# Kernel tuning notes

Hardware: AMD Instinct MI355X
Metric: run time of the kernel (lower is better)

## Reference

```python
import jax, jax.numpy as jnp
import numpy as np

B, L, D, H = 2, 2048, 1024, 16
DH = D // H  # 64


def setup_inputs() -> dict:
    key = jax.random.key(0)
    ks = jax.random.split(key, 11)
    s = 0.02
    return {
        "src": jax.random.normal(ks[0], (B, L, D), dtype=jnp.float32),
        "Wq": jax.random.normal(ks[1], (D, D), dtype=jnp.float32) * s,
        "bq": jax.random.normal(ks[2], (D,), dtype=jnp.float32) * s,
        "Wk": jax.random.normal(ks[3], (D, D), dtype=jnp.float32) * s,
        "bk": jax.random.normal(ks[4], (D,), dtype=jnp.float32) * s,
        "Wv": jax.random.normal(ks[5], (D, D), dtype=jnp.float32) * s,
        "bv": jax.random.normal(ks[6], (D,), dtype=jnp.float32) * s,
        "Wo": jax.random.normal(ks[7], (D, D), dtype=jnp.float32) * s,
        "bo": jax.random.normal(ks[8], (D,), dtype=jnp.float32) * s,
        "conv_w": jax.random.normal(ks[9], (H, D, 3), dtype=jnp.float32) * s,  # Conv1d weight [out=H, in=D, k=3]
        "conv_b": jax.random.normal(ks[10], (H,), dtype=jnp.float32) * s,
    }


def reference(src, Wq, bq, Wk, bk, Wv, bv, Wo, bo, conv_w, conv_b):
    b, l, d = src.shape
    h, dh = H, DH
    # QKV projections (torch Linear: x @ W.T + b), split into heads: [B,H,L,DH]
    Q = (src @ Wq.T + bq).reshape(b, l, h, dh).transpose(0, 2, 1, 3)
    K = (src @ Wk.T + bk).reshape(b, l, h, dh).transpose(0, 2, 1, 3)
    V = (src @ Wv.T + bv).reshape(b, l, h, dh).transpose(0, 2, 1, 3)
    # saliency conv: Conv1d(D->H, k=3, padding='same') on [B,D,L] -> [B,H,L]
    sal = jax.lax.conv_general_dilated(
        src.transpose(0, 2, 1), conv_w,
        window_strides=(1,), padding=[(1, 1)],
        dimension_numbers=("NCH", "OIH", "NCH"),
    ) + conv_b[None, :, None]
    # attention scores + per-head saliency bias (broadcast over query axis)
    scores = jnp.einsum("bhqd,bhkd->bhqk", Q, K) / jnp.sqrt(jnp.float32(dh))
    scores = scores + sal[:, :, None, :]
    attn = jax.nn.softmax(scores, axis=-1)  # dropout is identity in eval
    out = jnp.einsum("bhqk,bhkd->bhqd", attn, V)  # [B,H,L,DH]
    out = out.transpose(0, 2, 1, 3).reshape(b, l, d)
    out = out @ Wo.T + bo
    return out, attn
```

## Files before the change

kernel.cpp:

```cpp
#include <hip/hip_runtime.h>

typedef __bf16 bf16x8 __attribute__((ext_vector_type(8)));
typedef float f32x4 __attribute__((ext_vector_type(4)));
typedef unsigned short u16;
typedef unsigned int u32;

#define MFMA(a, b, c) __builtin_amdgcn_mfma_f32_16x16x32_bf16((a), (b), (c), 0, 0, 0)


__device__ __forceinline__ u16 f2bf(float f) {
  u32 u = __float_as_uint(f);
  return (u16)((u + 0x7fffu + ((u >> 16) & 1u)) >> 16);
}

__global__ __launch_bounds__(256) void cvt_bf16(const float4* __restrict__ x,
                                                uint2* __restrict__ y, int n4) {
  int i = blockIdx.x * 256 + threadIdx.x;
  if (i >= n4) return;
  float4 v = x[i];
  uint2 o;
  o.x = (u32)f2bf(v.x) | ((u32)f2bf(v.y) << 16);
  o.y = (u32)f2bf(v.z) | ((u32)f2bf(v.w) << 16);
  y[i] = o;
}

__global__ __launch_bounds__(256) void prep_cw(const float* __restrict__ cw,
                                               float* __restrict__ cwT) {
  int i = blockIdx.x * 256 + threadIdx.x;
  if (i >= 16 * 3 * 1024) return;
  int h = i / 3072;
  int j = (i - h * 3072) >> 10;
  int d = i & 1023;
  cwT[i] = cw[(h * 1024 + d) * 3 + j];
}

__global__ __launch_bounds__(256) void conv_sal_k(const float* __restrict__ src,
                                                  const float* __restrict__ cwT,
                                                  const float* __restrict__ cb,
                                                  float* __restrict__ sal) {
  const int t = threadIdx.x;
  const int h = t & 15, li = t >> 4;
  const int b = blockIdx.y;
  const int l = blockIdx.x * 16 + li;
  float acc = cb[h];
#pragma unroll
  for (int j = 0; j < 3; j++) {
    int ls = l + j - 1;
    if (ls < 0 || ls >= 2048) continue;
    const float4* sp = (const float4*)(src + ((size_t)b * 2048 + ls) * 1024);
    const float4* wp = (const float4*)(cwT + (h * 3 + j) * 1024);
    float s = 0.f;
    for (int d = 0; d < 256; d++) {
      float4 a = sp[d], w = wp[d];
      s += a.x * w.x + a.y * w.y + a.z * w.z + a.w * w.w;
    }
    acc += s;
  }
  sal[(b * 16 + h) * 2048 + l] = acc;
}

__global__ __launch_bounds__(256) void qkv_gemm(
    const u16* __restrict__ Xb, const u16* __restrict__ Wqb, const u16* __restrict__ Wkb,
    const u16* __restrict__ Wvb, const float* __restrict__ bq, const float* __restrict__ bk,
    const float* __restrict__ bv, u16* __restrict__ Qb, u16* __restrict__ Kb,
    u16* __restrict__ Vt) {
  const int seg = blockIdx.x >> 3;
  const u16* __restrict__ W = (seg == 0) ? Wqb : (seg == 1) ? Wkb : Wvb;
  const float* __restrict__ bias = (seg == 0) ? bq : (seg == 1) ? bk : bv;
  const int lane = threadIdx.x & 63, wid = threadIdx.x >> 6;
  const int cl = lane & 15, gp = lane >> 4;
  const int m0 = blockIdx.y * 128 + (wid >> 1) * 64;
  const int n0 = (blockIdx.x & 7) * 128 + (wid & 1) * 64;
  const u16* Xp = Xb + (size_t)(m0 + cl) * 1024 + gp * 8;
  const u16* Wp = W + (size_t)(n0 + cl) * 1024 + gp * 8;
  f32x4 acc[4][4] = {};
  for (int k = 0; k < 1024; k += 32) {
    bf16x8 a[4], b[4];
#pragma unroll
    for (int t = 0; t < 4; t++) {
      a[t] = *(const bf16x8*)(Xp + t * 16 * 1024 + k);
      b[t] = *(const bf16x8*)(Wp + t * 16 * 1024 + k);
    }
#pragma unroll
    for (int tm = 0; tm < 4; tm++)
#pragma unroll
      for (int tn = 0; tn < 4; tn++) acc[tm][tn] = MFMA(a[tm], b[tn], acc[tm][tn]);
  }
#pragma unroll
  for (int tn = 0; tn < 4; tn++) {
    int col = n0 + tn * 16 + cl;
    float bv_ = bias[col];
    int hh = col >> 6, dh = col & 63;
#pragma unroll
    for (int tm = 0; tm < 4; tm++) {
#pragma unroll
      for (int r = 0; r < 4; r++) {
        int row = m0 + tm * 16 + gp * 4 + r;
        u16 hv = f2bf(acc[tm][tn][r] + bv_);
        int bb = row >> 11, l = row & 2047;
        if (seg == 0)
          Qb[(((size_t)(bb * 16 + hh) * 2048 + l) << 6) + dh] = hv;
        else if (seg == 1)
          Kb[(((size_t)(bb * 16 + hh) * 2048 + l) << 6) + dh] = hv;
        else
          Vt[((size_t)(bb * 16 + hh) * 64 + dh) * 2048 + l] = hv;
      }
    }
  }
}

__global__ __launch_bounds__(256) void out_gemm(const u16* __restrict__ Xb,
                                                const u16* __restrict__ W,
                                                const float* __restrict__ bias,
                                                float* __restrict__ Y) {
  const int lane = threadIdx.x & 63, wid = threadIdx.x >> 6;
  const int cl = lane & 15, gp = lane >> 4;
  const int m0 = blockIdx.y * 128 + (wid >> 1) * 64;
  const int n0 = blockIdx.x * 128 + (wid & 1) * 64;
  const u16* Xp = Xb + (size_t)(m0 + cl) * 1024 + gp * 8;
  const u16* Wp = W + (size_t)(n0 + cl) * 1024 + gp * 8;
  f32x4 acc[4][4] = {};
  for (int k = 0; k < 1024; k += 32) {
    bf16x8 a[4], b[4];
#pragma unroll
    for (int t = 0; t < 4; t++) {
      a[t] = *(const bf16x8*)(Xp + t * 16 * 1024 + k);
      b[t] = *(const bf16x8*)(Wp + t * 16 * 1024 + k);
    }
#pragma unroll
    for (int tm = 0; tm < 4; tm++)
#pragma unroll
      for (int tn = 0; tn < 4; tn++) acc[tm][tn] = MFMA(a[tm], b[tn], acc[tm][tn]);
  }
#pragma unroll
  for (int tn = 0; tn < 4; tn++) {
    int col = n0 + tn * 16 + cl;
    float bv_ = bias[col];
#pragma unroll
    for (int tm = 0; tm < 4; tm++)
#pragma unroll
      for (int r = 0; r < 4; r++) {
        int row = m0 + tm * 16 + gp * 4 + r;
        Y[(size_t)row * 1024 + col] = acc[tm][tn][r] + bv_;
      }
  }
}

__global__ __launch_bounds__(256) void flash1(const u16* __restrict__ Qb,
                                              const u16* __restrict__ Kb,
                                              const u16* __restrict__ Vt,
                                              const float* __restrict__ sal,
                                              float* __restrict__ mrow,
                                              float* __restrict__ invl,
                                              u16* __restrict__ Ob) {
  __shared__ __align__(16) u16 pbuf[4][16][72];
  const int bh = blockIdx.x;
  const int b = bh >> 4, h = bh & 15;
  const int lane = threadIdx.x & 63, wid = threadIdx.x >> 6;
  const int cl = lane & 15, gp = lane >> 4;
  const int q0 = blockIdx.y * 64 + wid * 16;
  const u16* Qh = Qb + (size_t)bh * 2048 * 64;
  const u16* Kh = Kb + (size_t)bh * 2048 * 64;
  const u16* Vh = Vt + (size_t)bh * 64 * 2048;
  const float* salh = sal + bh * 2048;
  bf16x8 aQ0 = *(const bf16x8*)(Qh + (size_t)(q0 + cl) * 64 + gp * 8);
  bf16x8 aQ1 = *(const bf16x8*)(Qh + (size_t)(q0 + cl) * 64 + 32 + gp * 8);
  f32x4 oacc[4] = {};
  float m[4], l[4];
#pragma unroll
  for (int r = 0; r < 4; r++) { m[r] = -1e30f; l[r] = 0.f; }
  u16* pw = &pbuf[wid][0][0];
  for (int kb = 0; kb < 2048; kb += 64) {
    f32x4 st[4];
#pragma unroll
    for (int tn = 0; tn < 4; tn++) {
      const u16* kp = Kh + (size_t)(kb + tn * 16 + cl) * 64 + gp * 8;
      f32x4 s = {};
      s = MFMA(aQ0, *(const bf16x8*)kp, s);
      s = MFMA(aQ1, *(const bf16x8*)(kp + 32), s);
      st[tn] = s;
    }
#pragma unroll
    for (int tn = 0; tn < 4; tn++) {
      float sv = salh[kb + tn * 16 + cl];
#pragma unroll
      for (int r = 0; r < 4; r++) st[tn][r] = st[tn][r] * 0.125f + sv;
    }
    float mn[4], alpha[4];
#pragma unroll
    for (int r = 0; r < 4; r++) {
      float v = fmaxf(fmaxf(st[0][r], st[1][r]), fmaxf(st[2][r], st[3][r]));
      v = fmaxf(v, __shfl_xor(v, 1));
      v = fmaxf(v, __shfl_xor(v, 2));
      v = fmaxf(v, __shfl_xor(v, 4));
      v = fmaxf(v, __shfl_xor(v, 8));
      mn[r] = fmaxf(m[r], v);
      alpha[r] = __expf(m[r] - mn[r]);
      m[r] = mn[r];
    }
#pragma unroll
    for (int r = 0; r < 4; r++) {
      float s0 = 0.f;
#pragma unroll
      for (int tn = 0; tn < 4; tn++) {
        float p = __expf(st[tn][r] - mn[r]);
        st[tn][r] = p;
        s0 += p;
      }
      s0 += __shfl_xor(s0, 1);
      s0 += __shfl_xor(s0, 2);
      s0 += __shfl_xor(s0, 4);
      s0 += __shfl_xor(s0, 8);
      l[r] = l[r] * alpha[r] + s0;
#pragma unroll
      for (int tn = 0; tn < 4; tn++) oacc[tn][r] *= alpha[r];
    }
#pragma unroll
    for (int tn = 0; tn < 4; tn++)
#pragma unroll
      for (int r = 0; r < 4; r++) pw[(gp * 4 + r) * 72 + tn * 16 + cl] = f2bf(st[tn][r]);
    __syncthreads();
    bf16x8 aP0 = *(const bf16x8*)(pw + cl * 72 + gp * 8);
    bf16x8 aP1 = *(const bf16x8*)(pw + cl * 72 + 32 + gp * 8);
#pragma unroll
    for (int tn = 0; tn < 4; tn++) {
      const u16* vp = Vh + (size_t)(tn * 16 + cl) * 2048 + kb + gp * 8;
      oacc[tn] = MFMA(aP0, *(const bf16x8*)vp, oacc[tn]);
      oacc[tn] = MFMA(aP1, *(const bf16x8*)(vp + 32), oacc[tn]);
    }
    __syncthreads();
  }
  float inv[4];
#pragma unroll
  for (int r = 0; r < 4; r++) inv[r] = 1.0f / l[r];
#pragma unroll
  for (int tn = 0; tn < 4; tn++) {
    int d = h * 64 + tn * 16 + cl;
#pragma unroll
    for (int r = 0; r < 4; r++) {
      int q = q0 + gp * 4 + r;
      Ob[((size_t)(b * 2048 + q)) * 1024 + d] = f2bf(oacc[tn][r] * inv[r]);
    }
  }
  if (cl == 0) {
#pragma unroll
    for (int r = 0; r < 4; r++) {
      int q = q0 + gp * 4 + r;
      mrow[bh * 2048 + q] = m[r];
      invl[bh * 2048 + q] = inv[r];
    }
  }
}

__global__ __launch_bounds__(256) void attn_write(const u16* __restrict__ Qb,
                                                  const u16* __restrict__ Kb,
                                                  const float* __restrict__ sal,
                                                  const float* __restrict__ mrow,
                                                  const float* __restrict__ invl,
                                                  float* __restrict__ attn) {
  const int bh = blockIdx.x;
  const int lane = threadIdx.x & 63, wid = threadIdx.x >> 6;
  const int cl = lane & 15, gp = lane >> 4;
  const int q0 = blockIdx.y * 64 + wid * 16;
  const u16* Qh = Qb + (size_t)bh * 2048 * 64;
  const u16* Kh = Kb + (size_t)bh * 2048 * 64;
  const float* salh = sal + bh * 2048;
  bf16x8 aQ0 = *(const bf16x8*)(Qh + (size_t)(q0 + cl) * 64 + gp * 8);
  bf16x8 aQ1 = *(const bf16x8*)(Qh + (size_t)(q0 + cl) * 64 + 32 + gp * 8);
  float m[4], il[4];
#pragma unroll
  for (int r = 0; r < 4; r++) {
    int q = q0 + gp * 4 + r;
    m[r] = mrow[bh * 2048 + q];
    il[r] = invl[bh * 2048 + q];
  }
  float* arow = attn + (size_t)bh * 2048 * 2048;
  for (int kb = 0; kb < 2048; kb += 64) {
    f32x4 st[4];
#pragma unroll
    for (int tn = 0; tn < 4; tn++) {
      const u16* kp = Kh + (size_t)(kb + tn * 16 + cl) * 64 + gp * 8;
      f32x4 s = {};
      s = MFMA(aQ0, *(const bf16x8*)kp, s);
      s = MFMA(aQ1, *(const bf16x8*)(kp + 32), s);
      st[tn] = s;
    }
#pragma unroll
    for (int tn = 0; tn < 4; tn++) {
      float sv = salh[kb + tn * 16 + cl];
#pragma unroll
      for (int r = 0; r < 4; r++) {
        int q = q0 + gp * 4 + r;
        float p = __expf(st[tn][r] * 0.125f + sv - m[r]) * il[r];
        arow[(size_t)q * 2048 + kb + tn * 16 + cl] = p;
      }
    }
  }
}

extern "C" void kernel_launch(void* const* d_in, const int* in_sizes, int n_in,
                              void* d_out, int out_size, void* d_ws, size_t ws_size,
                              hipStream_t stream) {
  const float* src = (const float*)d_in[0];
  const float* Wq = (const float*)d_in[1];
  const float* bq = (const float*)d_in[2];
  const float* Wk = (const float*)d_in[3];
  const float* bk = (const float*)d_in[4];
  const float* Wv = (const float*)d_in[5];
  const float* bv = (const float*)d_in[6];
  const float* Wo = (const float*)d_in[7];
  const float* bo = (const float*)d_in[8];
  const float* cw = (const float*)d_in[9];
  const float* cb = (const float*)d_in[10];

  char* ws = (char*)d_ws;
  u16* srcb = (u16*)(ws + 0);
  u16* wqb = (u16*)(ws + 8388608);
  u16* wkb = (u16*)(ws + 10485760);
  u16* wvb = (u16*)(ws + 12582912);
  u16* wob = (u16*)(ws + 14680064);
  u16* Qb = (u16*)(ws + 16777216);
  u16* Kb = (u16*)(ws + 25165824);
  u16* Vt = (u16*)(ws + 33554432);
  u16* Ob = (u16*)(ws + 41943040);
  float* cwT = (float*)(ws + 50331648);
  float* sal = (float*)(ws + 50528256);
  float* mrow = (float*)(ws + 50790400);
  float* invl = (float*)(ws + 51052544);

  float* outp = (float*)d_out;
  float* attn = (float*)d_out + 4194304;

  cvt_bf16<<<4096, 256, 0, stream>>>((const float4*)src, (uint2*)srcb, 1048576);
  cvt_bf16<<<1024, 256, 0, stream>>>((const float4*)Wq, (uint2*)wqb, 262144);
  cvt_bf16<<<1024, 256, 0, stream>>>((const float4*)Wk, (uint2*)wkb, 262144);
  cvt_bf16<<<1024, 256, 0, stream>>>((const float4*)Wv, (uint2*)wvb, 262144);
  cvt_bf16<<<1024, 256, 0, stream>>>((const float4*)Wo, (uint2*)wob, 262144);
  prep_cw<<<192, 256, 0, stream>>>(cw, cwT);
  conv_sal_k<<<dim3(128, 2), 256, 0, stream>>>(src, cwT, cb, sal);
  qkv_gemm<<<dim3(24, 32), 256, 0, stream>>>(srcb, wqb, wkb, wvb, bq, bk, bv, Qb, Kb, Vt);
  flash1<<<dim3(32, 32), 256, 0, stream>>>(Qb, Kb, Vt, sal, mrow, invl, Ob);
  attn_write<<<dim3(32, 32), 256, 0, stream>>>(Qb, Kb, sal, mrow, invl, attn);
  out_gemm<<<dim3(8, 32), 256, 0, stream>>>(Ob, wob, bo, outp);
}
```

Before: 1.164 ms.

## Fuse prep kernels, stage GEMM tiles in LDS, merge flash and attn-write passes

Merges the five bf16 conversion kernels and the conv-weight transpose into one launch. The QKV and output GEMMs now load tiles cooperatively into shared memory instead of each wave reading global memory directly. The two attention kernels become one two-pass kernel: the first pass finds row max and sum, the second writes normalized attention and accumulates P·V, which drops one QK pass and the mrow/invl round trip. The conv accumulator is also split into four lanes; the GEMM LDS staging adds two barriers per k-step with no double buffering.

```diff
diff --git a/kernel.cpp b/kernel.cpp
--- a/kernel.cpp
+++ b/kernel.cpp
@@ -13,25 +13,35 @@
   return (u16)((u + 0x7fffu + ((u >> 16) & 1u)) >> 16);
 }
 
-__global__ __launch_bounds__(256) void cvt_bf16(const float4* __restrict__ x,
-                                                uint2* __restrict__ y, int n4) {
-  int i = blockIdx.x * 256 + threadIdx.x;
-  if (i >= n4) return;
-  float4 v = x[i];
-  uint2 o;
-  o.x = (u32)f2bf(v.x) | ((u32)f2bf(v.y) << 16);
-  o.y = (u32)f2bf(v.z) | ((u32)f2bf(v.w) << 16);
-  y[i] = o;
-}
-
-__global__ __launch_bounds__(256) void prep_cw(const float* __restrict__ cw,
-                                               float* __restrict__ cwT) {
-  int i = blockIdx.x * 256 + threadIdx.x;
-  if (i >= 16 * 3 * 1024) return;
-  int h = i / 3072;
-  int j = (i - h * 3072) >> 10;
-  int d = i & 1023;
-  cwT[i] = cw[(h * 1024 + d) * 3 + j];
+__global__ __launch_bounds__(256) void prep_all(
+    const float4* __restrict__ src, const float4* __restrict__ wq,
+    const float4* __restrict__ wk, const float4* __restrict__ wv,
+    const float4* __restrict__ wo, const float* __restrict__ cw,
+    uint2* __restrict__ srcb, uint2* __restrict__ wqb, uint2* __restrict__ wkb,
+    uint2* __restrict__ wvb, uint2* __restrict__ wob, float* __restrict__ cwT) {
+  int bx = blockIdx.x;
+  if (bx < 8192) {
+    const float4* in;
+    uint2* out;
+    int base;
+    if (bx < 4096) { in = src; out = srcb; base = 0; }
+    else if (bx < 5120) { in = wq; out = wqb; base = 4096; }
+    else if (bx < 6144) { in = wk; out = wkb; base = 5120; }
+    else if (bx < 7168) { in = wv; out = wvb; base = 6144; }
+    else { in = wo; out = wob; base = 7168; }
+    int i = (bx - base) * 256 + threadIdx.x;
+    float4 v = in[i];
+    uint2 o;
+    o.x = (u32)f2bf(v.x) | ((u32)f2bf(v.y) << 16);
+    o.y = (u32)f2bf(v.z) | ((u32)f2bf(v.w) << 16);
+    out[i] = o;
+  } else {
+    int i = (bx - 8192) * 256 + threadIdx.x;
+    int h = i / 3072;
+    int j = (i - h * 3072) >> 10;
+    int d = i & 1023;
+    cwT[i] = cw[(h * 1024 + d) * 3 + j];
+  }
 }
 
 __global__ __launch_bounds__(256) void conv_sal_k(const float* __restrict__ src,
@@ -42,21 +52,59 @@
   const int h = t & 15, li = t >> 4;
   const int b = blockIdx.y;
   const int l = blockIdx.x * 16 + li;
-  float acc = cb[h];
+  float4 acc = {0.f, 0.f, 0.f, 0.f};
 #pragma unroll
   for (int j = 0; j < 3; j++) {
     int ls = l + j - 1;
     if (ls < 0 || ls >= 2048) continue;
     const float4* sp = (const float4*)(src + ((size_t)b * 2048 + ls) * 1024);
     const float4* wp = (const float4*)(cwT + (h * 3 + j) * 1024);
-    float s = 0.f;
     for (int d = 0; d < 256; d++) {
       float4 a = sp[d], w = wp[d];
-      s += a.x * w.x + a.y * w.y + a.z * w.z + a.w * w.w;
-    }
-    acc += s;
-  }
-  sal[(b * 16 + h) * 2048 + l] = acc;
+      acc.x += a.x * w.x;
+      acc.y += a.y * w.y;
+      acc.z += a.z * w.z;
+      acc.w += a.w * w.w;
+    }
+  }
+  sal[(b * 16 + h) * 2048 + l] = cb[h] + ((acc.x + acc.y) + (acc.z + acc.w));
+}
+
+__device__ __forceinline__ void gemm_core(const u16* __restrict__ Xg, const u16* __restrict__ Wg,
+                                          int mblk, int nblk, u16* smA, u16* smB,
+                                          f32x4 acc[4][4]) {
+  const int t = threadIdx.x;
+  const int lane = t & 63, wid = t >> 6;
+  const int cl = lane & 15, gp = lane >> 4;
+  const int r0 = t >> 2, cc = (t & 3) * 8;
+  const u16* gA0 = Xg + (size_t)(mblk + r0) * 1024 + cc;
+  const u16* gB0 = Wg + (size_t)(nblk + r0) * 1024 + cc;
+  u16* lA0 = smA + t * 8;
+  u16* lB0 = smB + t * 8;
+  const u16* rA = smA + ((wid >> 1) * 64 + cl) * 32 + gp * 8;
+  const u16* rB = smB + ((wid & 1) * 64 + cl) * 32 + gp * 8;
+  for (int k0 = 0; k0 < 1024; k0 += 32) {
+    bf16x8 sa0 = *(const bf16x8*)(gA0 + k0);
+    bf16x8 sa1 = *(const bf16x8*)(gA0 + 64 * 1024 + k0);
+    bf16x8 sb0 = *(const bf16x8*)(gB0 + k0);
+    bf16x8 sb1 = *(const bf16x8*)(gB0 + 64 * 1024 + k0);
+    __syncthreads();
+    *(bf16x8*)lA0 = sa0;
+    *(bf16x8*)(lA0 + 2048) = sa1;
+    *(bf16x8*)lB0 = sb0;
+    *(bf16x8*)(lB0 + 2048) = sb1;
+    __syncthreads();
+    bf16x8 a[4], b[4];
+#pragma unroll
+    for (int i = 0; i < 4; i++) {
+      a[i] = *(const bf16x8*)(rA + i * 512);
+      b[i] = *(const bf16x8*)(rB + i * 512);
+    }
+#pragma unroll
+    for (int tm = 0; tm < 4; tm++)
+#pragma unroll
+      for (int tn = 0; tn < 4; tn++) acc[tm][tn] = MFMA(a[tm], b[tn], acc[tm][tn]);
+  }
 }
 
 __global__ __launch_bounds__(256) void qkv_gemm(
@@ -64,28 +112,17 @@
     const u16* __restrict__ Wvb, const float* __restrict__ bq, const float* __restrict__ bk,
     const float* __restrict__ bv, u16* __restrict__ Qb, u16* __restrict__ Kb,
     u16* __restrict__ Vt) {
+  __shared__ __align__(16) u16 smA[4096], smB[4096];
   const int seg = blockIdx.x >> 3;
   const u16* __restrict__ W = (seg == 0) ? Wqb : (seg == 1) ? Wkb : Wvb;
   const float* __restrict__ bias = (seg == 0) ? bq : (seg == 1) ? bk : bv;
   const int lane = threadIdx.x & 63, wid = threadIdx.x >> 6;
   const int cl = lane & 15, gp = lane >> 4;
-  const int m0 = blockIdx.y * 128 + (wid >> 1) * 64;
-  const int n0 = (blockIdx.x & 7) * 128 + (wid & 1) * 64;
-  const u16* Xp = Xb + (size_t)(m0 + cl) * 1024 + gp * 8;
-  const u16* Wp = W + (size_t)(n0 + cl) * 1024 + gp * 8;
+  const int mblk = blockIdx.y * 128, nblk = (blockIdx.x & 7) * 128;
+  const int m0 = mblk + (wid >> 1) * 64;
+  const int n0 = nblk + (wid & 1) * 64;
   f32x4 acc[4][4] = {};
-  for (int k = 0; k < 1024; k += 32) {
-    bf16x8 a[4], b[4];
-#pragma unroll
-    for (int t = 0; t < 4; t++) {
-      a[t] = *(const bf16x8*)(Xp + t * 16 * 1024 + k);
-      b[t] = *(const bf16x8*)(Wp + t * 16 * 1024 + k);
-    }
-#pragma unroll
-    for (int tm = 0; tm < 4; tm++)
-#pragma unroll
-      for (int tn = 0; tn < 4; tn++) acc[tm][tn] = MFMA(a[tm], b[tn], acc[tm][tn]);
-  }
+  gemm_core(Xb, W, mblk, nblk, smA, smB, acc);
 #pragma unroll
   for (int tn = 0; tn < 4; tn++) {
     int col = n0 + tn * 16 + cl;
@@ -113,25 +150,14 @@
                                                 const u16* __restrict__ W,
                                                 const float* __restrict__ bias,
                                                 float* __restrict__ Y) {
+  __shared__ __align__(16) u16 smA[4096], smB[4096];
   const int lane = threadIdx.x & 63, wid = threadIdx.x >> 6;
   const int cl = lane & 15, gp = lane >> 4;
-  const int m0 = blockIdx.y * 128 + (wid >> 1) * 64;
-  const int n0 = blockIdx.x * 128 + (wid & 1) * 64;
-  const u16* Xp = Xb + (size_t)(m0 + cl) * 1024 + gp * 8;
-  const u16* Wp = W + (size_t)(n0 + cl) * 1024 + gp * 8;
+  const int mblk = blockIdx.y * 128, nblk = blockIdx.x * 128;
+  const int m0 = mblk + (wid >> 1) * 64;
+  const int n0 = nblk + (wid & 1) * 64;
   f32x4 acc[4][4] = {};
-  for (int k = 0; k < 1024; k += 32) {
-    bf16x8 a[4], b[4];
-#pragma unroll
-    for (int t = 0; t < 4; t++) {
-      a[t] = *(const bf16x8*)(Xp + t * 16 * 1024 + k);
-      b[t] = *(const bf16x8*)(Wp + t * 16 * 1024 + k);
-    }
-#pragma unroll
-    for (int tm = 0; tm < 4; tm++)
-#pragma unroll
-      for (int tn = 0; tn < 4; tn++) acc[tm][tn] = MFMA(a[tm], b[tn], acc[tm][tn]);
-  }
+  gemm_core(Xb, W, mblk, nblk, smA, smB, acc);
 #pragma unroll
   for (int tn = 0; tn < 4; tn++) {
     int col = n0 + tn * 16 + cl;
@@ -146,13 +172,12 @@
   }
 }
 
-__global__ __launch_bounds__(256) void flash1(const u16* __restrict__ Qb,
-                                              const u16* __restrict__ Kb,
-                                              const u16* __restrict__ Vt,
-                                              const float* __restrict__ sal,
-                                              float* __restrict__ mrow,
-                                              float* __restrict__ invl,
-                                              u16* __restrict__ Ob) {
+__global__ __launch_bounds__(256) void flash_fused(const u16* __restrict__ Qb,
+                                                   const u16* __restrict__ Kb,
+                                                   const u16* __restrict__ Vt,
+                                                   const float* __restrict__ sal,
+                                                   float* __restrict__ attn,
+                                                   u16* __restrict__ Ob) {
   __shared__ __align__(16) u16 pbuf[4][16][72];
   const int bh = blockIdx.x;
   const int b = bh >> 4, h = bh & 15;
@@ -165,11 +190,10 @@
   const float* salh = sal + bh * 2048;
   bf16x8 aQ0 = *(const bf16x8*)(Qh + (size_t)(q0 + cl) * 64 + gp * 8);
   bf16x8 aQ1 = *(const bf16x8*)(Qh + (size_t)(q0 + cl) * 64 + 32 + gp * 8);
-  f32x4 oacc[4] = {};
   float m[4], l[4];
 #pragma unroll
   for (int r = 0; r < 4; r++) { m[r] = -1e30f; l[r] = 0.f; }
-  u16* pw = &pbuf[wid][0][0];
+
   for (int kb = 0; kb < 2048; kb += 64) {
     f32x4 st[4];
 #pragma unroll
@@ -186,7 +210,6 @@
 #pragma unroll
       for (int r = 0; r < 4; r++) st[tn][r] = st[tn][r] * 0.125f + sv;
     }
-    float mn[4], alpha[4];
 #pragma unroll
     for (int r = 0; r < 4; r++) {
       float v = fmaxf(fmaxf(st[0][r], st[1][r]), fmaxf(st[2][r], st[3][r]));
@@ -194,87 +217,26 @@
       v = fmaxf(v, __shfl_xor(v, 2));
       v = fmaxf(v, __shfl_xor(v, 4));
       v = fmaxf(v, __shfl_xor(v, 8));
-      mn[r] = fmaxf(m[r], v);
-      alpha[r] = __expf(m[r] - mn[r]);
-      m[r] = mn[r];
-    }
-#pragma unroll
-    for (int r = 0; r < 4; r++) {
+      float mn = fmaxf(m[r], v);
+      float alpha = __expf(m[r] - mn);
+      m[r] = mn;
       float s0 = 0.f;
 #pragma unroll
-      for (int tn = 0; tn < 4; tn++) {
-        float p = __expf(st[tn][r] - mn[r]);
-        st[tn][r] = p;
-        s0 += p;
-      }
+      for (int tn = 0; tn < 4; tn++) s0 += __expf(st[tn][r] - mn);
       s0 += __shfl_xor(s0, 1);
       s0 += __shfl_xor(s0, 2);
       s0 += __shfl_xor(s0, 4);
       s0 += __shfl_xor(s0, 8);
-      l[r] = l[r] * alpha[r] + s0;
-#pragma unroll
-      for (int tn = 0; tn < 4; tn++) oacc[tn][r] *= alpha[r];
-    }
-#pragma unroll
-    for (int tn = 0; tn < 4; tn++)
-#pragma unroll
-      for (int r = 0; r < 4; r++) pw[(gp * 4 + r) * 72 + tn * 16 + cl] = f2bf(st[tn][r]);
-    __syncthreads();
-    bf16x8 aP0 = *(const bf16x8*)(pw + cl * 72 + gp * 8);
-    bf16x8 aP1 = *(const bf16x8*)(pw + cl * 72 + 32 + gp * 8);
-#pragma unroll
-    for (int tn = 0; tn < 4; tn++) {
-      const u16* vp = Vh + (size_t)(tn * 16 + cl) * 2048 + kb + gp * 8;
-      oacc[tn] = MFMA(aP0, *(const bf16x8*)vp, oacc[tn]);
-      oacc[tn] = MFMA(aP1, *(const bf16x8*)(vp + 32), oacc[tn]);
-    }
-    __syncthreads();
-  }
-  float inv[4];
-#pragma unroll
-  for (int r = 0; r < 4; r++) inv[r] = 1.0f / l[r];
-#pragma unroll
-  for (int tn = 0; tn < 4; tn++) {
-    int d = h * 64 + tn * 16 + cl;
-#pragma unroll
-    for (int r = 0; r < 4; r++) {
-      int q = q0 + gp * 4 + r;
-      Ob[((size_t)(b * 2048 + q)) * 1024 + d] = f2bf(oacc[tn][r] * inv[r]);
-    }
-  }
-  if (cl == 0) {
-#pragma unroll
-    for (int r = 0; r < 4; r++) {
-      int q = q0 + gp * 4 + r;
-      mrow[bh * 2048 + q] = m[r];
-      invl[bh * 2048 + q] = inv[r];
-    }
-  }
-}
-
-__global__ __launch_bounds__(256) void attn_write(const u16* __restrict__ Qb,
-                                                  const u16* __restrict__ Kb,
-                                                  const float* __restrict__ sal,
-                                                  const float* __restrict__ mrow,
-                                                  const float* __restrict__ invl,
-                                                  float* __restrict__ attn) {
-  const int bh = blockIdx.x;
-  const int lane = threadIdx.x & 63, wid = threadIdx.x >> 6;
-  const int cl = lane & 15, gp = lane >> 4;
-  const int q0 = blockIdx.y * 64 + wid * 16;
-  const u16* Qh = Qb + (size_t)bh * 2048 * 64;
-  const u16* Kh = Kb + (size_t)bh * 2048 * 64;
-  const float* salh = sal + bh * 2048;
-  bf16x8 aQ0 = *(const bf16x8*)(Qh + (size_t)(q0 + cl) * 64 + gp * 8);
-  bf16x8 aQ1 = *(const bf16x8*)(Qh + (size_t)(q0 + cl) * 64 + 32 + gp * 8);
-  float m[4], il[4];
-#pragma unroll
-  for (int r = 0; r < 4; r++) {
-    int q = q0 + gp * 4 + r;
-    m[r] = mrow[bh * 2048 + q];
-    il[r] = invl[bh * 2048 + q];
-  }
+      l[r] = l[r] * alpha + s0;
+    }
+  }
+  float il[4];
+#pragma unroll
+  for (int r = 0; r < 4; r++) il[r] = 1.0f / l[r];
+
+  f32x4 oacc[4] = {};
   float* arow = attn + (size_t)bh * 2048 * 2048;
+  u16* pw = &pbuf[wid][0][0];
   for (int kb = 0; kb < 2048; kb += 64) {
     f32x4 st[4];
 #pragma unroll
@@ -290,10 +252,29 @@
       float sv = salh[kb + tn * 16 + cl];
 #pragma unroll
       for (int r = 0; r < 4; r++) {
-        int q = q0 + gp * 4 + r;
-        float p = __expf(st[tn][r] * 0.125f + sv - m[r]) * il[r];
-        arow[(size_t)q * 2048 + kb + tn * 16 + cl] = p;
+        float p = __expf(st[tn][r] * 0.125f + sv - m[r]);
+        arow[(size_t)(q0 + gp * 4 + r) * 2048 + kb + tn * 16 + cl] = p * il[r];
+        pw[(gp * 4 + r) * 72 + tn * 16 + cl] = f2bf(p);
       }
+    }
+    __syncthreads();
+    bf16x8 aP0 = *(const bf16x8*)(pw + cl * 72 + gp * 8);
+    bf16x8 aP1 = *(const bf16x8*)(pw + cl * 72 + 32 + gp * 8);
+#pragma unroll
+    for (int tn = 0; tn < 4; tn++) {
+      const u16* vp = Vh + (size_t)(tn * 16 + cl) * 2048 + kb + gp * 8;
+      oacc[tn] = MFMA(aP0, *(const bf16x8*)vp, oacc[tn]);
+      oacc[tn] = MFMA(aP1, *(const bf16x8*)(vp + 32), oacc[tn]);
+    }
+    __syncthreads();
+  }
+#pragma unroll
+  for (int tn = 0; tn < 4; tn++) {
+    int d = h * 64 + tn * 16 + cl;
+#pragma unroll
+    for (int r = 0; r < 4; r++) {
+      int q = q0 + gp * 4 + r;
+      Ob[((size_t)(b * 2048 + q)) * 1024 + d] = f2bf(oacc[tn][r] * il[r]);
     }
   }
 }
@@ -325,21 +306,16 @@
   u16* Ob = (u16*)(ws + 41943040);
   float* cwT = (float*)(ws + 50331648);
   float* sal = (float*)(ws + 50528256);
-  float* mrow = (float*)(ws + 50790400);
-  float* invl = (float*)(ws + 51052544);
 
   float* outp = (float*)d_out;
   float* attn = (float*)d_out + 4194304;
 
-  cvt_bf16<<<4096, 256, 0, stream>>>((const float4*)src, (uint2*)srcb, 1048576);
-  cvt_bf16<<<1024, 256, 0, stream>>>((const float4*)Wq, (uint2*)wqb, 262144);
-  cvt_bf16<<<1024, 256, 0, stream>>>((const float4*)Wk, (uint2*)wkb, 262144);
-  cvt_bf16<<<1024, 256, 0, stream>>>((const float4*)Wv, (uint2*)wvb, 262144);
-  cvt_bf16<<<1024, 256, 0, stream>>>((const float4*)Wo, (uint2*)wob, 262144);
-  prep_cw<<<192, 256, 0, stream>>>(cw, cwT);
+  prep_all<<<8384, 256, 0, stream>>>((const float4*)src, (const float4*)Wq, (const float4*)Wk,
+                                     (const float4*)Wv, (const float4*)Wo, cw,
+                                     (uint2*)srcb, (uint2*)wqb, (uint2*)wkb, (uint2*)wvb,
+                                     (uint2*)wob, cwT);
   conv_sal_k<<<dim3(128, 2), 256, 0, stream>>>(src, cwT, cb, sal);
   qkv_gemm<<<dim3(24, 32), 256, 0, stream>>>(srcb, wqb, wkb, wvb, bq, bk, bv, Qb, Kb, Vt);
-  flash1<<<dim3(32, 32), 256, 0, stream>>>(Qb, Kb, Vt, sal, mrow, invl, Ob);
-  attn_write<<<dim3(32, 32), 256, 0, stream>>>(Qb, Kb, sal, mrow, invl, attn);
+  flash_fused<<<dim3(32, 32), 256, 0, stream>>>(Qb, Kb, Vt, sal, attn, Ob);
   out_gemm<<<dim3(8, 32), 256, 0, stream>>>(Ob, wob, bo, outp);
 }
```

After: 1.078 ms. 1.08x faster.
